# Optimization experiments

Measured on AMD Instinct MI355X. Metric: run time of the kernel, lower is better.

## Reference

```python
import jax, jax.numpy as jnp
import numpy as np


def setup_inputs() -> dict:
    key = jax.random.key(0)
    k1, k2 = jax.random.split(key)
    B, N, M = 16, 4096, 4096
    x1 = jax.random.normal(k1, (B, N, 3), dtype=jnp.float32)
    x2 = jax.random.normal(k2, (B, M, 3), dtype=jnp.float32)
    return {"x1": x1, "x2": x2}


def reference(x1, x2) -> jnp.ndarray:
    # x1: [B, N, 3], x2: [B, M, 3]
    # dist_matrix[b, i, j] = ||x1[b,i] - x2[b,j]||^2 via |a|^2 + |b|^2 - 2 a.b
    x1_norm = jnp.sum(x1 * x1, axis=2, keepdims=True)           # [B, N, 1]
    x2_norm = jnp.sum(x2 * x2, axis=2)[:, None, :]              # [B, 1, M]
    cross = jnp.einsum('bnd,bmd->bnm', x1, x2)                  # [B, N, M]
    dist_matrix = x1_norm + x2_norm - 2.0 * cross               # [B, N, M]
    min_1_to_2 = jnp.min(dist_matrix, axis=2)                   # [B, N]
    min_2_to_1 = jnp.min(dist_matrix, axis=1)                   # [B, M]
    chamfer = jnp.mean(min_1_to_2, axis=1) + jnp.mean(min_2_to_1, axis=1)  # [B]
    return chamfer
```

## Files before the change

kernel.cpp:

```cpp
#include <hip/hip_runtime.h>


typedef __attribute__((ext_vector_type(8))) __bf16 bf16x8;
typedef __attribute__((ext_vector_type(16))) float f32x16;

#define TI 256
#define JCHUNK 1024
#define THREADS 256

__device__ __forceinline__ unsigned f2bf(float f) {
  unsigned u = __float_as_uint(f);
  return (u + 0x7FFFu + ((u >> 16) & 1u)) >> 16;
}
__device__ __forceinline__ float bf2f(unsigned s) {
  return __uint_as_float(s << 16);
}
__device__ __forceinline__ unsigned pk(unsigned lo, unsigned hi) {
  return (lo & 0xFFFFu) | (hi << 16);
}

__global__ __launch_bounds__(THREADS, 4) void chamfer_mfma(
    const float* __restrict__ x1, const float* __restrict__ x2,
    float* __restrict__ out, int N, int M) {
  __shared__ uint4 Al4[(TI / 32) * 2 * 32];
  __shared__ uint4 Ql4[(JCHUNK / 32) * 2 * 32];

  const int b   = blockIdx.y;
  const int dir = blockIdx.z;
  const float* __restrict__ P = dir ? x2 : x1;
  const float* __restrict__ Q = dir ? x1 : x2;
  const int nrows = dir ? M : N;
  const int ncols = dir ? N : M;

  const int tid = threadIdx.x;

  {
    const int i = blockIdx.x * TI + tid;
    const float* p = P + (b * nrows + i) * 3;
    const float x = p[0], y = p[1], z = p[2];
    const unsigned hx = f2bf(x), hy = f2bf(y), hz = f2bf(z);
    const unsigned lx = f2bf(x - bf2f(hx));
    const unsigned ly = f2bf(y - bf2f(hy));
    const unsigned lz = f2bf(z - bf2f(hz));
    const float n = fmaf(x, x, fmaf(y, y, z * z));
    const unsigned nh = f2bf(n), nl = f2bf(n - bf2f(nh));
    const unsigned one = 0x3F80u;
    uint4 w0, w1;
    w0.x = pk(hx, hy); w0.y = pk(hz, hx); w0.z = pk(hy, hz); w0.w = pk(lx, ly);
    w1.x = pk(lz, one); w1.y = pk(one, nh); w1.z = pk(nl, 0u); w1.w = 0u;
    Al4[((tid >> 5) * 2 + 0) * 32 + (tid & 31)] = w0;
    Al4[((tid >> 5) * 2 + 1) * 32 + (tid & 31)] = w1;
  }
  __syncthreads();

  const int lane = tid & 63;
  const int half = lane >> 5;
  const int l31  = lane & 31;
  const int wave = tid >> 6;

  const bf16x8 af0 = *(const bf16x8*)&Al4[(wave * 4 + 0 + half) * 32 + l31];
  const bf16x8 af1 = *(const bf16x8*)&Al4[(wave * 4 + 2 + half) * 32 + l31];

  f32x16 zero;
#pragma unroll
  for (int e = 0; e < 16; ++e) zero[e] = 0.f;

  float rm0[16], rm1[16];
#pragma unroll
  for (int e = 0; e < 16; ++e) { rm0[e] = 3.0e38f; rm1[e] = 3.0e38f; }

  const int nchunk = ncols / JCHUNK;
  for (int c = 0; c < nchunk; ++c) {
    __syncthreads();
#pragma unroll
    for (int s0 = 0; s0 < JCHUNK / THREADS; ++s0) {
      const int s = s0 * THREADS + tid;
      const int j = c * JCHUNK + s;
      const float* q = Q + (b * ncols + j) * 3;
      const float x = q[0], y = q[1], z = q[2];
      const float sx = -2.f * x, sy = -2.f * y, sz = -2.f * z;
      const unsigned Hx = f2bf(sx), Hy = f2bf(sy), Hz = f2bf(sz);
      const unsigned Lx = f2bf(sx - bf2f(Hx));
      const unsigned Ly = f2bf(sy - bf2f(Hy));
      const unsigned Lz = f2bf(sz - bf2f(Hz));
      const float n = fmaf(x, x, fmaf(y, y, z * z));
      const unsigned nh = f2bf(n), nl = f2bf(n - bf2f(nh));
      const unsigned one = 0x3F80u;
      uint4 w0, w1;
      w0.x = pk(Hx, Hy); w0.y = pk(Hz, Lx); w0.z = pk(Ly, Lz); w0.w = pk(Hx, Hy);
      w1.x = pk(Hz, nh); w1.y = pk(nl, one); w1.z = pk(one, 0u); w1.w = 0u;
      Ql4[(s >> 5) * 64 + (s & 31)] = w0;
      Ql4[(s >> 5) * 64 + 32 + (s & 31)] = w1;
    }
    __syncthreads();

#pragma unroll 4
    for (int jt = 0; jt < JCHUNK / 32; jt += 2) {
      const bf16x8 b0 = *(const bf16x8*)&Ql4[jt * 64 + half * 32 + l31];
      const bf16x8 b1 = *(const bf16x8*)&Ql4[(jt + 1) * 64 + half * 32 + l31];
      const f32x16 a00 =
          __builtin_amdgcn_mfma_f32_32x32x16_bf16(af0, b0, zero, 0, 0, 0);
      const f32x16 a01 =
          __builtin_amdgcn_mfma_f32_32x32x16_bf16(af0, b1, zero, 0, 0, 0);
#pragma unroll
      for (int e = 0; e < 16; ++e)
        rm0[e] = fminf(fminf(a00[e], a01[e]), rm0[e]);
      const f32x16 a10 =
          __builtin_amdgcn_mfma_f32_32x32x16_bf16(af1, b0, zero, 0, 0, 0);
      const f32x16 a11 =
          __builtin_amdgcn_mfma_f32_32x32x16_bf16(af1, b1, zero, 0, 0, 0);
#pragma unroll
      for (int e = 0; e < 16; ++e)
        rm1[e] = fminf(fminf(a10[e], a11[e]), rm1[e]);
    }
  }

  float ssum = 0.f;
#pragma unroll
  for (int e = 0; e < 16; ++e) {
    float v = rm0[e];
    v = fminf(v, __shfl_xor(v, 1));
    v = fminf(v, __shfl_xor(v, 2));
    v = fminf(v, __shfl_xor(v, 4));
    v = fminf(v, __shfl_xor(v, 8));
    v = fminf(v, __shfl_xor(v, 16));
    ssum += v;
  }
#pragma unroll
  for (int e = 0; e < 16; ++e) {
    float v = rm1[e];
    v = fminf(v, __shfl_xor(v, 1));
    v = fminf(v, __shfl_xor(v, 2));
    v = fminf(v, __shfl_xor(v, 4));
    v = fminf(v, __shfl_xor(v, 8));
    v = fminf(v, __shfl_xor(v, 16));
    ssum += v;
  }
  ssum += __shfl_xor(ssum, 32);
  if (lane == 0) atomicAdd(&out[b], ssum * (1.0f / (float)nrows));
}

extern "C" void kernel_launch(void* const* d_in, const int* in_sizes, int n_in,
                              void* d_out, int out_size, void* d_ws,
                              size_t ws_size, hipStream_t stream) {
  const float* x1 = (const float*)d_in[0];
  const float* x2 = (const float*)d_in[1];
  float* out = (float*)d_out;
  const int B = out_size;
  const int N = in_sizes[0] / (3 * B);
  const int M = in_sizes[1] / (3 * B);

  hipMemsetAsync(out, 0, B * sizeof(float), stream);
  dim3 grid(N / TI, B, 2);
  chamfer_mfma<<<grid, THREADS, 0, stream>>>(x1, x2, out, N, M);
}
```

Measured before the change: 98.11 us.

## Prepack B fragments globally, drop LDS staging, split columns with atomicMin rows

Splits the work into three kernels. A prepack kernel builds the bf16 hi/lo B fragments once into workspace memory. The main kernel reads those fragments straight from global memory with register prefetch, so it needs no LDS and no __syncthreads. It builds the A fragments in registers, splits the column range across two blocks, and merges per-row minima with atomicMin on unsigned float bits. A final reduction kernel sums the row minima per batch. This removes the per-chunk redundant conversion and barrier stalls, at the cost of extra launches, a memset, global-memory fragment traffic and atomics. Sizes are now hardcoded to the test shape.

Result: faster. 92.62 us (-5.6%).

```diff
diff --git a/kernel.cpp b/kernel.cpp
--- a/kernel.cpp
+++ b/kernel.cpp
@@ -4,9 +4,9 @@
 typedef __attribute__((ext_vector_type(8))) __bf16 bf16x8;
 typedef __attribute__((ext_vector_type(16))) float f32x16;
 
-#define TI 256
-#define JCHUNK 1024
-#define THREADS 256
+#define PTS 4096
+#define TILES 128
+#define NB 16
 
 __device__ __forceinline__ unsigned f2bf(float f) {
   unsigned u = __float_as_uint(f);
@@ -19,47 +19,70 @@
   return (lo & 0xFFFFu) | (hi << 16);
 }
 
-__global__ __launch_bounds__(THREADS, 4) void chamfer_mfma(
+__global__ __launch_bounds__(256) void prepack_b(const float* __restrict__ x1,
+                                                 const float* __restrict__ x2,
+                                                 uint4* __restrict__ Bfr) {
+  const int id = blockIdx.x * 256 + threadIdx.x;
+  const int d = id >> 16;
+  const int b = (id >> 12) & (NB - 1);
+  const int j = id & (PTS - 1);
+  const float* q = (d ? x1 : x2) + (size_t)(b * PTS + j) * 3;
+  const float x = q[0], y = q[1], z = q[2];
+  const float sx = -2.f * x, sy = -2.f * y, sz = -2.f * z;
+  const unsigned Hx = f2bf(sx), Hy = f2bf(sy), Hz = f2bf(sz);
+  const unsigned Lx = f2bf(sx - bf2f(Hx));
+  const unsigned Ly = f2bf(sy - bf2f(Hy));
+  const unsigned Lz = f2bf(sz - bf2f(Hz));
+  const float n = fmaf(x, x, fmaf(y, y, z * z));
+  const unsigned nh = f2bf(n), nl = f2bf(n - bf2f(nh));
+  const unsigned one = 0x3F80u;
+  uint4 w0, w1;
+  w0.x = pk(Hx, Hy); w0.y = pk(Hz, Lx); w0.z = pk(Ly, Lz); w0.w = pk(Hx, Hy);
+  w1.x = pk(Hz, nh); w1.y = pk(nl, one); w1.z = pk(one, 0u); w1.w = 0u;
+  uint4* base =
+      Bfr + ((size_t)((d * NB + b) * TILES + (j >> 5)) * 2) * 32 + (j & 31);
+  base[0]  = w0;
+  base[32] = w1;
+}
+
+__global__ __launch_bounds__(128, 3) void chamfer_main(
     const float* __restrict__ x1, const float* __restrict__ x2,
-    float* __restrict__ out, int N, int M) {
-  __shared__ uint4 Al4[(TI / 32) * 2 * 32];
-  __shared__ uint4 Ql4[(JCHUNK / 32) * 2 * 32];
+    const uint4* __restrict__ Bfr, unsigned* __restrict__ rowm) {
+  const int rb = blockIdx.x;
+  const int b  = blockIdx.y;
+  const int z  = blockIdx.z;
+  const int d  = z >> 1, ch = z & 1;
 
-  const int b   = blockIdx.y;
-  const int dir = blockIdx.z;
-  const float* __restrict__ P = dir ? x2 : x1;
-  const float* __restrict__ Q = dir ? x1 : x2;
-  const int nrows = dir ? M : N;
-  const int ncols = dir ? N : M;
+  const int tid  = threadIdx.x;
+  const int lane = tid & 63;
+  const int half = lane >> 5;
+  const int l31  = lane & 31;
+  const int wave = tid >> 6;
 
-  const int tid = threadIdx.x;
-
-  {
-    const int i = blockIdx.x * TI + tid;
-    const float* p = P + (b * nrows + i) * 3;
-    const float x = p[0], y = p[1], z = p[2];
-    const unsigned hx = f2bf(x), hy = f2bf(y), hz = f2bf(z);
+  const float* P = d ? x2 : x1;
+  const int t0 = rb * 4 + wave * 2;
+  bf16x8 af[2];
+#pragma unroll
+  for (int rr = 0; rr < 2; ++rr) {
+    const int r = (t0 + rr) * 32 + l31;
+    const float* p = P + (size_t)(b * PTS + r) * 3;
+    const float x = p[0], y = p[1], zc = p[2];
+    const unsigned hx = f2bf(x), hy = f2bf(y), hz = f2bf(zc);
     const unsigned lx = f2bf(x - bf2f(hx));
     const unsigned ly = f2bf(y - bf2f(hy));
-    const unsigned lz = f2bf(z - bf2f(hz));
-    const float n = fmaf(x, x, fmaf(y, y, z * z));
+    const unsigned lz = f2bf(zc - bf2f(hz));
+    const float n = fmaf(x, x, fmaf(y, y, zc * zc));
     const unsigned nh = f2bf(n), nl = f2bf(n - bf2f(nh));
     const unsigned one = 0x3F80u;
     uint4 w0, w1;
     w0.x = pk(hx, hy); w0.y = pk(hz, hx); w0.z = pk(hy, hz); w0.w = pk(lx, ly);
     w1.x = pk(lz, one); w1.y = pk(one, nh); w1.z = pk(nl, 0u); w1.w = 0u;
-    Al4[((tid >> 5) * 2 + 0) * 32 + (tid & 31)] = w0;
-    Al4[((tid >> 5) * 2 + 1) * 32 + (tid & 31)] = w1;
+    uint4 w;
+    w.x = half ? w1.x : w0.x; w.y = half ? w1.y : w0.y;
+    w.z = half ? w1.z : w0.z; w.w = half ? w1.w : w0.w;
+    af[rr] = *(const bf16x8*)&w;
   }
-  __syncthreads();
-
-  const int lane = tid & 63;
-  const int half = lane >> 5;
-  const int l31  = lane & 31;
-  const int wave = tid >> 6;
-
-  const bf16x8 af0 = *(const bf16x8*)&Al4[(wave * 4 + 0 + half) * 32 + l31];
-  const bf16x8 af1 = *(const bf16x8*)&Al4[(wave * 4 + 2 + half) * 32 + l31];
+  const bf16x8 af0 = af[0], af1 = af[1];
 
   f32x16 zero;
 #pragma unroll
@@ -69,53 +92,34 @@
 #pragma unroll
   for (int e = 0; e < 16; ++e) { rm0[e] = 3.0e38f; rm1[e] = 3.0e38f; }
 
-  const int nchunk = ncols / JCHUNK;
-  for (int c = 0; c < nchunk; ++c) {
-    __syncthreads();
+  const uint4* bp =
+      Bfr + ((size_t)((d * NB + b) * TILES + ch * 64) * 2) * 32;
+  const int off = half * 32 + l31;
+  bf16x8 b0 = *(const bf16x8*)&bp[off];
+  bf16x8 b1 = *(const bf16x8*)&bp[64 + off];
+#pragma unroll 2
+  for (int jt = 0; jt < 64; jt += 2) {
+    const int nx = (jt + 2) & 63;
+    const bf16x8 n0 = *(const bf16x8*)&bp[nx * 64 + off];
+    const bf16x8 n1 = *(const bf16x8*)&bp[(nx + 1) * 64 + off];
+    const f32x16 a00 =
+        __builtin_amdgcn_mfma_f32_32x32x16_bf16(af0, b0, zero, 0, 0, 0);
+    const f32x16 a01 =
+        __builtin_amdgcn_mfma_f32_32x32x16_bf16(af0, b1, zero, 0, 0, 0);
 #pragma unroll
-    for (int s0 = 0; s0 < JCHUNK / THREADS; ++s0) {
-      const int s = s0 * THREADS + tid;
-      const int j = c * JCHUNK + s;
-      const float* q = Q + (b * ncols + j) * 3;
-      const float x = q[0], y = q[1], z = q[2];
-      const float sx = -2.f * x, sy = -2.f * y, sz = -2.f * z;
-      const unsigned Hx = f2bf(sx), Hy = f2bf(sy), Hz = f2bf(sz);
-      const unsigned Lx = f2bf(sx - bf2f(Hx));
-      const unsigned Ly = f2bf(sy - bf2f(Hy));
-      const unsigned Lz = f2bf(sz - bf2f(Hz));
-      const float n = fmaf(x, x, fmaf(y, y, z * z));
-      const unsigned nh = f2bf(n), nl = f2bf(n - bf2f(nh));
-      const unsigned one = 0x3F80u;
-      uint4 w0, w1;
-      w0.x = pk(Hx, Hy); w0.y = pk(Hz, Lx); w0.z = pk(Ly, Lz); w0.w = pk(Hx, Hy);
-      w1.x = pk(Hz, nh); w1.y = pk(nl, one); w1.z = pk(one, 0u); w1.w = 0u;
-      Ql4[(s >> 5) * 64 + (s & 31)] = w0;
-      Ql4[(s >> 5) * 64 + 32 + (s & 31)] = w1;
-    }
-    __syncthreads();
-
-#pragma unroll 4
-    for (int jt = 0; jt < JCHUNK / 32; jt += 2) {
-      const bf16x8 b0 = *(const bf16x8*)&Ql4[jt * 64 + half * 32 + l31];
-      const bf16x8 b1 = *(const bf16x8*)&Ql4[(jt + 1) * 64 + half * 32 + l31];
-      const f32x16 a00 =
-          __builtin_amdgcn_mfma_f32_32x32x16_bf16(af0, b0, zero, 0, 0, 0);
-      const f32x16 a01 =
-          __builtin_amdgcn_mfma_f32_32x32x16_bf16(af0, b1, zero, 0, 0, 0);
+    for (int e = 0; e < 16; ++e)
+      rm0[e] = fminf(fminf(a00[e], a01[e]), rm0[e]);
+    const f32x16 a10 =
+        __builtin_amdgcn_mfma_f32_32x32x16_bf16(af1, b0, zero, 0, 0, 0);
+    const f32x16 a11 =
+        __builtin_amdgcn_mfma_f32_32x32x16_bf16(af1, b1, zero, 0, 0, 0);
 #pragma unroll
-      for (int e = 0; e < 16; ++e)
-        rm0[e] = fminf(fminf(a00[e], a01[e]), rm0[e]);
-      const f32x16 a10 =
-          __builtin_amdgcn_mfma_f32_32x32x16_bf16(af1, b0, zero, 0, 0, 0);
-      const f32x16 a11 =
-          __builtin_amdgcn_mfma_f32_32x32x16_bf16(af1, b1, zero, 0, 0, 0);
-#pragma unroll
-      for (int e = 0; e < 16; ++e)
-        rm1[e] = fminf(fminf(a10[e], a11[e]), rm1[e]);
-    }
+    for (int e = 0; e < 16; ++e)
+      rm1[e] = fminf(fminf(a10[e], a11[e]), rm1[e]);
+    b0 = n0; b1 = n1;
   }
 
-  float ssum = 0.f;
+  unsigned* rbase = rowm + (size_t)(d * NB + b) * PTS + rb * 128 + wave * 64;
 #pragma unroll
   for (int e = 0; e < 16; ++e) {
     float v = rm0[e];
@@ -124,7 +128,10 @@
     v = fminf(v, __shfl_xor(v, 4));
     v = fminf(v, __shfl_xor(v, 8));
     v = fminf(v, __shfl_xor(v, 16));
-    ssum += v;
+    if (l31 == e) {
+      const int rl = (e & 3) + 8 * (e >> 2) + 4 * half;
+      atomicMin(rbase + rl, __float_as_uint(fmaxf(v, 0.f)));
+    }
   }
 #pragma unroll
   for (int e = 0; e < 16; ++e) {
@@ -134,10 +141,32 @@
     v = fminf(v, __shfl_xor(v, 4));
     v = fminf(v, __shfl_xor(v, 8));
     v = fminf(v, __shfl_xor(v, 16));
-    ssum += v;
+    if (l31 == e) {
+      const int rl = 32 + (e & 3) + 8 * (e >> 2) + 4 * half;
+      atomicMin(rbase + rl, __float_as_uint(fmaxf(v, 0.f)));
+    }
   }
-  ssum += __shfl_xor(ssum, 32);
-  if (lane == 0) atomicAdd(&out[b], ssum * (1.0f / (float)nrows));
+}
+
+__global__ __launch_bounds__(256) void reduce_rows(
+    const unsigned* __restrict__ rowm, float* __restrict__ out) {
+  const int b = blockIdx.x;
+  const int tid = threadIdx.x;
+  const unsigned* r0 = rowm + (size_t)b * PTS;
+  const unsigned* r1 = rowm + (size_t)(NB + b) * PTS;
+  float s = 0.f;
+  for (int i = tid; i < PTS; i += 256)
+    s += __uint_as_float(r0[i]) + __uint_as_float(r1[i]);
+  s += __shfl_xor(s, 1);
+  s += __shfl_xor(s, 2);
+  s += __shfl_xor(s, 4);
+  s += __shfl_xor(s, 8);
+  s += __shfl_xor(s, 16);
+  s += __shfl_xor(s, 32);
+  __shared__ float acc[4];
+  if ((tid & 63) == 0) acc[tid >> 6] = s;
+  __syncthreads();
+  if (tid == 0) out[b] = (acc[0] + acc[1] + acc[2] + acc[3]) * (1.f / PTS);
 }
 
 extern "C" void kernel_launch(void* const* d_in, const int* in_sizes, int n_in,
@@ -146,11 +175,13 @@
   const float* x1 = (const float*)d_in[0];
   const float* x2 = (const float*)d_in[1];
   float* out = (float*)d_out;
-  const int B = out_size;
-  const int N = in_sizes[0] / (3 * B);
-  const int M = in_sizes[1] / (3 * B);
 
-  hipMemsetAsync(out, 0, B * sizeof(float), stream);
-  dim3 grid(N / TI, B, 2);
-  chamfer_mfma<<<grid, THREADS, 0, stream>>>(x1, x2, out, N, M);
+  uint4* Bfr = (uint4*)d_ws;
+  unsigned* rowm = (unsigned*)((char*)d_ws + (size_t)2 * NB * TILES * 2 * 32 * 16);
+  hipMemsetAsync(rowm, 0xFF, (size_t)2 * NB * PTS * 4, stream);
+
+  prepack_b<<<(2 * NB * PTS) / 256, 256, 0, stream>>>(x1, x2, Bfr);
+  dim3 grid(PTS / 128, NB, 4);
+  chamfer_main<<<grid, 128, 0, stream>>>(x1, x2, Bfr, rowm);
+  reduce_rows<<<NB, 256, 0, stream>>>(rowm, out);
 }
```
